# Kernel tuning notes

Measured on AMD Instinct MI355X. Metric: run time of the kernel, lower is better.

The kernel has to match this reference:

```python
import jax, jax.numpy as jnp
import numpy as np

N = 262144      # total points
B = 128         # scenes (batch segments), 2048 points each
C_IN, C_MID, C_OUT = 256, 256, 512
SIGMA_EPS = 1e-4

def setup_inputs() -> dict:
    key = jax.random.key(0)
    k1, k2, k3, k4, k5 = jax.random.split(key, 5)
    pos = jax.random.normal(k1, (N, 3), dtype=jnp.float32)
    feature = jax.random.normal(k2, (N, C_IN), dtype=jnp.float32)
    batch = jnp.repeat(jnp.arange(B, dtype=jnp.int64), N // B)  # sorted segment ids, no empty segments
    W1 = jax.random.normal(k3, (C_IN + 3, C_MID), dtype=jnp.float32) * 0.02
    b1 = jnp.zeros((C_MID,), dtype=jnp.float32)
    W2 = jax.random.normal(k4, (C_MID, C_OUT), dtype=jnp.float32) * 0.02
    b2 = jnp.zeros((C_OUT,), dtype=jnp.float32)
    noise = jax.random.normal(k5, (B, C_OUT // 2), dtype=jnp.float32)  # reparam eps
    return {"pos": pos, "feature": feature, "batch": batch,
            "W1": W1, "b1": b1, "W2": W2, "b2": b2, "noise": noise}

def reference(pos, feature, batch, W1, b1, W2, b2, noise):
    # scatter_mean: per-scene centroid  [B,3]
    counts = jax.ops.segment_sum(jnp.ones((pos.shape[0],), pos.dtype), batch, num_segments=B)
    pos_center = jax.ops.segment_sum(pos, batch, num_segments=B) / counts[:, None]
    # PointConv with edges (i -> batch[i]): relative position gather
    rel = pos - pos_center[batch]                                  # [N,3]
    msg = jnp.concatenate([feature, rel], axis=1) @ W1 + b1        # [N, C_MID]
    msg = jax.nn.relu(msg)
    agg = jax.ops.segment_max(msg, batch, num_segments=B)          # [B, C_MID] (PointNetConv max aggr)
    out = agg @ W2 + b2                                            # [B, C_OUT]
    mu, sigma_raw = jnp.split(out, 2, axis=1)                      # [B,256] each
    sigma = jax.nn.softplus(sigma_raw) + SIGMA_EPS                 # to_sigma
    z_what_coarse = mu + sigma * noise                             # rsample
    return z_what_coarse
```

## Files before the change

### kernel.cpp

```cpp
#include <hip/hip_runtime.h>
#include <hip/hip_bf16.h>
#include <math.h>

#define PTS_PER 2048

typedef __attribute__((ext_vector_type(8))) short bf16x8;
typedef __attribute__((ext_vector_type(4))) float f32x4;

__device__ __forceinline__ unsigned int pk_bf16(float a, float b) {
    union { __hip_bfloat162 h; unsigned int u; } cv;
    cv.h = __float22bfloat162_rn(make_float2(a, b));
    return cv.u;
}

__device__ __forceinline__ unsigned short f2bf(float f) {
    union { __hip_bfloat16 h; unsigned short u; } cv;
    cv.h = __float2bfloat16(f);
    return cv.u;
}

__global__ __launch_bounds__(256) void prep_kernel(
    const float* __restrict__ pos, const float* __restrict__ W1,
    float* __restrict__ center, unsigned short* __restrict__ w1t) {
    int bid = blockIdx.x, t = threadIdx.x;
    if (bid < 128) {
        __shared__ float red[3 * 256];
        float sx = 0.f, sy = 0.f, sz = 0.f;
        int base = bid * PTS_PER;
        #pragma unroll
        for (int j = 0; j < 8; ++j) {
            int idx = base + j * 256 + t;
            sx += pos[idx * 3 + 0];
            sy += pos[idx * 3 + 1];
            sz += pos[idx * 3 + 2];
        }
        red[t] = sx; red[256 + t] = sy; red[512 + t] = sz;
        __syncthreads();
        for (int s = 128; s > 0; s >>= 1) {
            if (t < s) {
                red[t]       += red[t + s];
                red[256 + t] += red[256 + t + s];
                red[512 + t] += red[512 + t + s];
            }
            __syncthreads();
        }
        if (t == 0) {
            center[bid * 3 + 0] = red[0]   * (1.f / PTS_PER);
            center[bid * 3 + 1] = red[256] * (1.f / PTS_PER);
            center[bid * 3 + 2] = red[512] * (1.f / PTS_PER);
        }
    } else {
        int base = ((bid - 128) * 256 + t) * 4;
        int n = base >> 8, k0 = base & 255;
        #pragma unroll
        for (int j = 0; j < 4; ++j)
            w1t[n * 256 + k0 + j] = f2bf(W1[(k0 + j) * 256 + n]);
    }
}

__global__ __launch_bounds__(256, 3) void main_kernel(
    const float* __restrict__ feature, const float* __restrict__ pos,
    const float* __restrict__ W1, const float* __restrict__ center,
    const unsigned short* __restrict__ w1t, float* __restrict__ partial) {
    __shared__ unsigned short sA[64 * 264];
    __shared__ float sRel[64][3];

    int bid = blockIdx.x, t = threadIdx.x;
    int row0 = bid * 64;
    int scene = bid >> 5;

    if (t < 64) {
        int gr = row0 + t;
        sRel[t][0] = pos[gr * 3 + 0] - center[scene * 3 + 0];
        sRel[t][1] = pos[gr * 3 + 1] - center[scene * 3 + 1];
        sRel[t][2] = pos[gr * 3 + 2] - center[scene * 3 + 2];
    }

    int w = t >> 6, lane = t & 63, quad = lane >> 4, lo = lane & 15;
    const unsigned short* wbase = w1t + (size_t)(w * 64) * 256;

    bf16x8 bpre[4];
    {
        int kk = quad * 8;
        #pragma unroll
        for (int ct = 0; ct < 4; ++ct)
            bpre[ct] = *(const bf16x8*)(wbase + (ct * 16 + lo) * 256 + kk);
    }

    const float4* f4 = (const float4*)(feature + (size_t)row0 * 256);
    #pragma unroll
    for (int it = 0; it < 16; ++it) {
        int fidx = it * 256 + t;
        int row = fidx >> 6, c4 = fidx & 63;
        float4 v = f4[fidx];
        uint2 h = make_uint2(pk_bf16(v.x, v.y), pk_bf16(v.z, v.w));
        *(uint2*)(sA + row * 264 + c4 * 4) = h;
    }
    __syncthreads();

    f32x4 acc[4][4];
    #pragma unroll
    for (int rt = 0; rt < 4; ++rt)
        #pragma unroll
        for (int ct = 0; ct < 4; ++ct)
            acc[rt][ct] = (f32x4){0.f, 0.f, 0.f, 0.f};

    #pragma unroll
    for (int k0 = 0; k0 < 256; k0 += 32) {
        int kk = k0 + quad * 8;
        bf16x8 afr[4], bfr[4];
        #pragma unroll
        for (int rt = 0; rt < 4; ++rt)
            afr[rt] = *(const bf16x8*)(sA + (rt * 16 + lo) * 264 + kk);
        #pragma unroll
        for (int ct = 0; ct < 4; ++ct)
            bfr[ct] = (k0 == 0) ? bpre[ct]
                    : *(const bf16x8*)(wbase + (ct * 16 + lo) * 256 + kk);
        #pragma unroll
        for (int rt = 0; rt < 4; ++rt)
            #pragma unroll
            for (int ct = 0; ct < 4; ++ct)
                acc[rt][ct] = __builtin_amdgcn_mfma_f32_16x16x32_bf16(
                    afr[rt], bfr[ct], acc[rt][ct], 0, 0, 0);
    }

    const float* Wp = W1 + 256 * 256;
    #pragma unroll
    for (int ct = 0; ct < 4; ++ct) {
        int col = w * 64 + ct * 16 + lo;
        float wp0 = Wp[col], wp1 = Wp[256 + col], wp2 = Wp[512 + col];
        float m = -3.4e38f;
        #pragma unroll
        for (int rt = 0; rt < 4; ++rt) {
            #pragma unroll
            for (int r = 0; r < 4; ++r) {
                int row = rt * 16 + quad * 4 + r;
                float v = acc[rt][ct][r] + sRel[row][0] * wp0
                        + sRel[row][1] * wp1 + sRel[row][2] * wp2;
                m = fmaxf(m, v);
            }
        }
        m = fmaxf(m, __shfl_xor(m, 16, 64));
        m = fmaxf(m, __shfl_xor(m, 32, 64));
        if (quad == 0)
            partial[(size_t)bid * 256 + col] = m;
    }
}

__global__ __launch_bounds__(256) void final_kernel(
    const float* __restrict__ partial, const float* __restrict__ b1,
    const float* __restrict__ W2, const float* __restrict__ b2,
    const float* __restrict__ noise, float* __restrict__ out) {
    int s = blockIdx.x, t = threadIdx.x;
    __shared__ float sa[256];
    const float* p = partial + (size_t)s * 32 * 256;
    float m = -3.4e38f;
    #pragma unroll
    for (int c = 0; c < 32; ++c)
        m = fmaxf(m, p[c * 256 + t]);
    sa[t] = fmaxf(m + b1[t], 0.f);
    __syncthreads();
    float mu = b2[t], sr = b2[256 + t];
    #pragma unroll 8
    for (int k = 0; k < 256; ++k) {
        float a = sa[k];
        mu += a * W2[k * 512 + t];
        sr += a * W2[k * 512 + 256 + t];
    }
    float sp = (sr > 20.f) ? sr : log1pf(expf(sr));
    float sigma = sp + 1e-4f;
    out[s * 256 + t] = mu + sigma * noise[s * 256 + t];
}

extern "C" void kernel_launch(void* const* d_in, const int* in_sizes, int n_in,
                              void* d_out, int out_size, void* d_ws, size_t ws_size,
                              hipStream_t stream) {
    const float* pos     = (const float*)d_in[0];
    const float* feature = (const float*)d_in[1];
    const float* W1      = (const float*)d_in[3];
    const float* b1      = (const float*)d_in[4];
    const float* W2      = (const float*)d_in[5];
    const float* b2      = (const float*)d_in[6];
    const float* noise   = (const float*)d_in[7];
    float* out = (float*)d_out;

    char* ws = (char*)d_ws;
    float* partial        = (float*)ws;
    unsigned short* w1t   = (unsigned short*)(ws + (4 << 20));
    float* center         = (float*)(ws + (4 << 20) + 131072);

    prep_kernel <<<192, 256, 0, stream>>>(pos, W1, center, w1t);
    main_kernel <<<4096, 256, 0, stream>>>(feature, pos, W1, center, w1t, partial);
    final_kernel<<<128, 256, 0, stream>>>(partial, b1, W2, b2, noise, out);
}
```

Baseline: 421.3 us.

## Make main kernel persistent per half-scene with W1 resident in LDS

The main kernel drops from 4096 small blocks to 256 blocks of 512 threads, each covering 1024 points of one scene. The whole bf16 W1 is staged once into LDS and reused across 8 row iterations. Feature rows load straight into registers, with the next iteration's loads issued before the current MFMAs, and a running max is kept in registers. This is meant to cut redundant global weight reads and the per-block partial traffic. In exchange it uses large LDS (about 135KB), very high register pressure, and only 256 blocks, which may leave CUs underfilled on the 256-CU device.

Measured after the change: 923.4 us. 2.19x slower.

```diff
diff --git a/kernel.cpp b/kernel.cpp
--- a/kernel.cpp
+++ b/kernel.cpp
@@ -3,16 +3,18 @@
 #include <math.h>
 
 #define PTS_PER 2048
+#define LDSB 264
 
 typedef __attribute__((ext_vector_type(8))) short bf16x8;
 typedef __attribute__((ext_vector_type(4))) float f32x4;
+
+union BF8 { uint4 u; bf16x8 v; };
 
 __device__ __forceinline__ unsigned int pk_bf16(float a, float b) {
     union { __hip_bfloat162 h; unsigned int u; } cv;
     cv.h = __float22bfloat162_rn(make_float2(a, b));
     return cv.u;
 }
-
 __device__ __forceinline__ unsigned short f2bf(float f) {
     union { __hip_bfloat16 h; unsigned short u; } cv;
     cv.h = __float2bfloat16(f);
@@ -58,92 +60,122 @@
     }
 }
 
-__global__ __launch_bounds__(256, 3) void main_kernel(
+__global__ __launch_bounds__(512, 2) void main_kernel(
     const float* __restrict__ feature, const float* __restrict__ pos,
     const float* __restrict__ W1, const float* __restrict__ center,
     const unsigned short* __restrict__ w1t, float* __restrict__ partial) {
-    __shared__ unsigned short sA[64 * 264];
-    __shared__ float sRel[64][3];
-
-    int bid = blockIdx.x, t = threadIdx.x;
-    int row0 = bid * 64;
-    int scene = bid >> 5;
-
-    if (t < 64) {
-        int gr = row0 + t;
-        sRel[t][0] = pos[gr * 3 + 0] - center[scene * 3 + 0];
-        sRel[t][1] = pos[gr * 3 + 1] - center[scene * 3 + 1];
-        sRel[t][2] = pos[gr * 3 + 2] - center[scene * 3 + 2];
-    }
-
+    __shared__ unsigned short sB[256 * LDSB];
+    __shared__ float sRed[8][256];
+    __shared__ float sRel[8][16][4];
+
+    int t = threadIdx.x, blk = blockIdx.x;
     int w = t >> 6, lane = t & 63, quad = lane >> 4, lo = lane & 15;
-    const unsigned short* wbase = w1t + (size_t)(w * 64) * 256;
-
-    bf16x8 bpre[4];
+    int scene = blk >> 1;
+
+    float cx = center[scene * 3 + 0];
+    float cy = center[scene * 3 + 1];
+    float cz = center[scene * 3 + 2];
+
+    float4 apf[16];
     {
-        int kk = quad * 8;
-        #pragma unroll
-        for (int ct = 0; ct < 4; ++ct)
-            bpre[ct] = *(const bf16x8*)(wbase + (ct * 16 + lo) * 256 + kk);
-    }
-
-    const float4* f4 = (const float4*)(feature + (size_t)row0 * 256);
+        const float* arow = feature + ((size_t)blk * 1024 + w * 16 + lo) * 256;
+        #pragma unroll
+        for (int ks = 0; ks < 8; ++ks) {
+            apf[2 * ks]     = *(const float4*)(arow + ks * 32 + quad * 8);
+            apf[2 * ks + 1] = *(const float4*)(arow + ks * 32 + quad * 8 + 4);
+        }
+    }
+
     #pragma unroll
     for (int it = 0; it < 16; ++it) {
-        int fidx = it * 256 + t;
-        int row = fidx >> 6, c4 = fidx & 63;
-        float4 v = f4[fidx];
-        uint2 h = make_uint2(pk_bf16(v.x, v.y), pk_bf16(v.z, v.w));
-        *(uint2*)(sA + row * 264 + c4 * 4) = h;
+        int id = it * 512 + t;
+        int n = id >> 5, c = id & 31;
+        uint4 v = *(const uint4*)(w1t + n * 256 + c * 8);
+        *(uint4*)(sB + n * LDSB + c * 8) = v;
     }
     __syncthreads();
 
-    f32x4 acc[4][4];
+    const float* Wp = W1 + 256 * 256;
+    float rmax[16];
     #pragma unroll
-    for (int rt = 0; rt < 4; ++rt)
-        #pragma unroll
-        for (int ct = 0; ct < 4; ++ct)
-            acc[rt][ct] = (f32x4){0.f, 0.f, 0.f, 0.f};
-
-    #pragma unroll
-    for (int k0 = 0; k0 < 256; k0 += 32) {
-        int kk = k0 + quad * 8;
-        bf16x8 afr[4], bfr[4];
-        #pragma unroll
-        for (int rt = 0; rt < 4; ++rt)
-            afr[rt] = *(const bf16x8*)(sA + (rt * 16 + lo) * 264 + kk);
-        #pragma unroll
-        for (int ct = 0; ct < 4; ++ct)
-            bfr[ct] = (k0 == 0) ? bpre[ct]
-                    : *(const bf16x8*)(wbase + (ct * 16 + lo) * 256 + kk);
-        #pragma unroll
-        for (int rt = 0; rt < 4; ++rt)
+    for (int ct = 0; ct < 16; ++ct) rmax[ct] = -3.4e38f;
+
+    for (int iter = 0; iter < 8; ++iter) {
+        int rowBase = blk * 1024 + iter * 128 + w * 16;
+
+        BF8 abf[8];
+        #pragma unroll
+        for (int ks = 0; ks < 8; ++ks) {
+            float4 a = apf[2 * ks], b = apf[2 * ks + 1];
+            abf[ks].u = make_uint4(pk_bf16(a.x, a.y), pk_bf16(a.z, a.w),
+                                   pk_bf16(b.x, b.y), pk_bf16(b.z, b.w));
+        }
+
+        if (lane < 16) {
+            int gr = rowBase + lane;
+            sRel[w][lane][0] = pos[gr * 3 + 0] - cx;
+            sRel[w][lane][1] = pos[gr * 3 + 1] - cy;
+            sRel[w][lane][2] = pos[gr * 3 + 2] - cz;
+        }
+
+        if (iter < 7) {
+            const float* arow = feature + ((size_t)rowBase + 128 + lo) * 256;
             #pragma unroll
-            for (int ct = 0; ct < 4; ++ct)
-                acc[rt][ct] = __builtin_amdgcn_mfma_f32_16x16x32_bf16(
-                    afr[rt], bfr[ct], acc[rt][ct], 0, 0, 0);
-    }
-
-    const float* Wp = W1 + 256 * 256;
-    #pragma unroll
-    for (int ct = 0; ct < 4; ++ct) {
-        int col = w * 64 + ct * 16 + lo;
-        float wp0 = Wp[col], wp1 = Wp[256 + col], wp2 = Wp[512 + col];
-        float m = -3.4e38f;
-        #pragma unroll
-        for (int rt = 0; rt < 4; ++rt) {
+            for (int ks = 0; ks < 8; ++ks) {
+                apf[2 * ks]     = *(const float4*)(arow + ks * 32 + quad * 8);
+                apf[2 * ks + 1] = *(const float4*)(arow + ks * 32 + quad * 8 + 4);
+            }
+        }
+
+        f32x4 acc[16];
+        #pragma unroll
+        for (int ct = 0; ct < 16; ++ct) acc[ct] = (f32x4){0.f, 0.f, 0.f, 0.f};
+        #pragma unroll
+        for (int ks = 0; ks < 8; ++ks) {
+            int kk = ks * 32 + quad * 8;
+            #pragma unroll
+            for (int ct = 0; ct < 16; ++ct) {
+                bf16x8 bfr = *(const bf16x8*)(sB + (ct * 16 + lo) * LDSB + kk);
+                acc[ct] = __builtin_amdgcn_mfma_f32_16x16x32_bf16(
+                    abf[ks].v, bfr, acc[ct], 0, 0, 0);
+            }
+        }
+
+        float r0[4], r1[4], r2[4];
+        #pragma unroll
+        for (int r = 0; r < 4; ++r) {
+            int rr = quad * 4 + r;
+            r0[r] = sRel[w][rr][0];
+            r1[r] = sRel[w][rr][1];
+            r2[r] = sRel[w][rr][2];
+        }
+        #pragma unroll
+        for (int ct = 0; ct < 16; ++ct) {
+            int col = ct * 16 + lo;
+            float wp0 = Wp[col], wp1 = Wp[256 + col], wp2 = Wp[512 + col];
+            float m = rmax[ct];
             #pragma unroll
             for (int r = 0; r < 4; ++r) {
-                int row = rt * 16 + quad * 4 + r;
-                float v = acc[rt][ct][r] + sRel[row][0] * wp0
-                        + sRel[row][1] * wp1 + sRel[row][2] * wp2;
+                float v = acc[ct][r] + r0[r] * wp0 + r1[r] * wp1 + r2[r] * wp2;
                 m = fmaxf(m, v);
             }
-        }
+            rmax[ct] = m;
+        }
+    }
+
+    #pragma unroll
+    for (int ct = 0; ct < 16; ++ct) {
+        float m = rmax[ct];
         m = fmaxf(m, __shfl_xor(m, 16, 64));
         m = fmaxf(m, __shfl_xor(m, 32, 64));
-        if (quad == 0)
-            partial[(size_t)bid * 256 + col] = m;
+        if (quad == 0) sRed[w][ct * 16 + lo] = m;
+    }
+    __syncthreads();
+    if (t < 256) {
+        float m = sRed[0][t];
+        #pragma unroll
+        for (int ww = 1; ww < 8; ++ww) m = fmaxf(m, sRed[ww][t]);
+        partial[(size_t)blk * 256 + t] = m;
     }
 }
 
@@ -153,11 +185,8 @@
     const float* __restrict__ noise, float* __restrict__ out) {
     int s = blockIdx.x, t = threadIdx.x;
     __shared__ float sa[256];
-    const float* p = partial + (size_t)s * 32 * 256;
-    float m = -3.4e38f;
-    #pragma unroll
-    for (int c = 0; c < 32; ++c)
-        m = fmaxf(m, p[c * 256 + t]);
+    const float* p = partial + (size_t)s * 2 * 256;
+    float m = fmaxf(p[t], p[256 + t]);
     sa[t] = fmaxf(m + b1[t], 0.f);
     __syncthreads();
     float mu = b2[t], sr = b2[256 + t];
@@ -186,10 +215,10 @@
 
     char* ws = (char*)d_ws;
     float* partial        = (float*)ws;
-    unsigned short* w1t   = (unsigned short*)(ws + (4 << 20));
-    float* center         = (float*)(ws + (4 << 20) + 131072);
+    unsigned short* w1t   = (unsigned short*)(ws + 262144);
+    float* center         = (float*)(ws + 262144 + 131072);
 
     prep_kernel <<<192, 256, 0, stream>>>(pos, W1, center, w1t);
-    main_kernel <<<4096, 256, 0, stream>>>(feature, pos, W1, center, w1t, partial);
+    main_kernel <<<256, 512, 0, stream>>>(feature, pos, W1, center, w1t, partial);
     final_kernel<<<128, 256, 0, stream>>>(partial, b1, W2, b2, noise, out);
 }
```
